# Kernel tuning notes

Measured on AMD Instinct MI355X. Metric: run time of the kernel, lower is better.

The kernel has to match this reference:

```python
import jax, jax.numpy as jnp
import numpy as np

B, C, H, W = 32, 512, 32, 32
K, D = 1024, 512  # codebook_size, latent_dim


def setup_inputs() -> dict:
    key = jax.random.key(0)
    k1, k2 = jax.random.split(key)
    z = jax.random.normal(k1, (B, C, H, W), dtype=jnp.float32)
    # nn.Embedding weight init: uniform(-1/codebook_size, 1/codebook_size)
    codebook = jax.random.uniform(k2, (K, D), dtype=jnp.float32,
                                  minval=-1.0 / K, maxval=1.0 / K)
    return {"z": z, "codebook": codebook}


def reference(z, codebook):
    b, c, h, w = z.shape
    # [B, C, H, W] -> [B, H, W, C] -> [B*H*W, C]
    z_flat = jnp.transpose(z, (0, 2, 3, 1)).reshape(-1, c)
    # squared euclidean distances via ||z||^2 - 2 z.W^T + ||W||^2
    distances = (
        jnp.sum(z_flat * z_flat, axis=1, keepdims=True)
        - 2.0 * jnp.matmul(z_flat, codebook.T)
        + jnp.sum(codebook * codebook, axis=1)[None, :]
    )  # [B*H*W, K]
    min_indices = jnp.argmin(distances, axis=1)  # [B*H*W]
    # Faithful to the original: gather then reshape directly to z.shape
    # (no inverse permute), which works because C == latent_dim.
    quantized = codebook[min_indices].reshape(z.shape)
    return quantized, min_indices.reshape(b, -1)
```

## Files before the change

kernel.cpp:

```cpp
#include <hip/hip_runtime.h>
#include <hip/hip_bf16.h>

#define M_ROWS  32768
#define D_DIM   512
#define K_CODES 1024
#define HW      1024
#define IMG_STRIDE (D_DIM * HW)

#define WH_OFF   0u
#define A_OFF    1048576u
#define W_OFF    1179648u
#define PK_OFF   1183744u
#define PART_OFF 1312768u
#define WL1_OFF  3934208u
#define WL2_OFF  4065280u
#define CNT_OFF  4196352u

#define WINDOW 5.0e-4f

__device__ __forceinline__ float fmul32(float a, float b) {
  float r; asm volatile("v_mul_f32 %0, %1, %2" : "=v"(r) : "v"(a), "v"(b)); return r;
}
__device__ __forceinline__ float fadd32(float a, float b) {
  float r; asm volatile("v_add_f32 %0, %1, %2" : "=v"(r) : "v"(a), "v"(b)); return r;
}
__device__ __forceinline__ float pair8(const float* r) {
  return fadd32(fadd32(fadd32(r[0], r[1]), fadd32(r[2], r[3])),
                fadd32(fadd32(r[4], r[5]), fadd32(r[6], r[7])));
}

__device__ __forceinline__ unsigned short f2bf(float x) {
  __hip_bfloat16 h = __float2bfloat16(x);
  unsigned short u; __builtin_memcpy(&u, &h, 2); return u;
}

typedef __attribute__((ext_vector_type(8))) short b8;
typedef __attribute__((ext_vector_type(4))) float f4;

struct T3 { float s1, s2, s3; int n1, n2; };
__device__ __forceinline__ void t3_merge(T3& a, const T3& bb) {
  T3 x = a, y = bb;
  bool bf = (y.s1 < x.s1) || (y.s1 == x.s1 && y.n1 < x.n1);
  if (bf) { T3 t = x; x = y; y = t; }
  float rs2; int rn2; float rs3;
  bool c2 = (y.s1 < x.s2) || (y.s1 == x.s2 && y.n1 < x.n2);
  if (c2) { rs2 = y.s1; rn2 = y.n1; rs3 = fminf(x.s2, y.s2); }
  else    { rs2 = x.s2; rn2 = x.n2; rs3 = fminf(x.s3, y.s1); }
  a.s1 = x.s1; a.n1 = x.n1; a.s2 = rs2; a.n2 = rn2; a.s3 = rs3;
}

__global__ __launch_bounds__(256) void vq_prep(const float* __restrict__ z,
                                               float* __restrict__ A,
                                               char* __restrict__ zh_b) {
  __shared__ float zs[4][64 * 68];
  const int wave = threadIdx.x >> 6, t = threadIdx.x & 63;
  const int i0 = blockIdx.x * 256 + wave * 64;
  const int b = i0 >> 10, hw0 = i0 & 1023;
  const float* zbase = z + (size_t)b * IMG_STRIDE + hw0;
  float* zsw = zs[wave];
  const int pos = i0 + t;
  const size_t mbase = (size_t)(pos >> 4) * 1024 + (size_t)(pos & 15) * 16;
  float r8[8], blk[4];
  alignas(16) unsigned short hs[8];
#pragma unroll
  for (int ch = 0; ch < 8; ++ch) {
    __syncthreads();
    {
      const int l = t & 15, j0 = t >> 4;
#pragma unroll
      for (int jj = 0; jj < 16; ++jj) {
        int j = j0 * 16 + jj;
        float4 vv = *(const float4*)(zbase + (size_t)(ch * 64 + j) * HW + 4 * l);
        *(float4*)(zsw + j * 68 + 4 * l) = vv;
      }
    }
    __syncthreads();
#pragma unroll
    for (int j = 0; j < 64; ++j) {
      const int c = ch * 64 + j;
      float v = zsw[j * 68 + t];
      hs[j & 7] = f2bf(v);
      if ((j & 7) == 7) {
        const int kc = c >> 5, q = (c >> 3) & 3;
        *(uint4*)(zh_b + (size_t)kc * 2097152 + q * 256 + mbase) = *(uint4*)hs;
      }
      float pq = fmul32(v, v);
      const int k = c & 7, m = c & 127;
      if (m < 8) r8[k] = pq;
      else       r8[k] = fadd32(r8[k], pq);
      if (m == 127) blk[c >> 7] = pair8(r8);
    }
  }
  A[pos] = fadd32(fadd32(blk[0], blk[1]), fadd32(blk[2], blk[3]));
}

__global__ void vq_prepw(const float* __restrict__ cb, float* __restrict__ W,
                         char* __restrict__ wh_b, int* __restrict__ cnt) {
  if (blockIdx.x == 0 && threadIdx.x < 2) cnt[threadIdx.x] = 0;
  const int n = blockIdx.x * 256 + threadIdx.x;
  const float* wp = cb + (size_t)n * D_DIM;
  const size_t nbase = (size_t)(n >> 4) * 1024 + (size_t)(n & 15) * 16;
  float r8[8], blk[4];
  alignas(16) unsigned short hs[8];
#pragma unroll
  for (int bb = 0; bb < 4; ++bb) {
#pragma unroll
    for (int g = 0; g < 16; ++g) {
      float vv[8];
#pragma unroll
      for (int k = 0; k < 8; ++k) vv[k] = wp[bb * 128 + g * 8 + k];
#pragma unroll
      for (int k = 0; k < 8; ++k) {
        float pq = fmul32(vv[k], vv[k]);
        if (g == 0) r8[k] = pq;
        else        r8[k] = fadd32(r8[k], pq);
        hs[k] = f2bf(vv[k]);
      }
      const int kc = bb * 4 + (g >> 2), q = g & 3;
      *(uint4*)(wh_b + (size_t)kc * 65536 + q * 256 + nbase) = *(uint4*)hs;
    }
    blk[bb] = pair8(r8);
  }
  W[n] = fadd32(fadd32(blk[0], blk[1]), fadd32(blk[2], blk[3]));
}

__global__ __launch_bounds__(256, 2) void vq_score(
    const char* __restrict__ zh_b, const char* __restrict__ wh_b,
    const float* __restrict__ Wws, float* __restrict__ part)
{
  __shared__ float red[1280];
  const int tid = threadIdx.x;
  const int lane = tid & 63, wave = tid >> 6;
  const int wr = wave >> 1, wc = wave & 1;
  const int bm = blockIdx.x & 255, bn = blockIdx.x >> 8;
  const int m0 = bm * 128, n0 = bn * 256;

  f4 acc[4][8];
#pragma unroll
  for (int r = 0; r < 4; ++r)
#pragma unroll
    for (int v = 0; v < 8; ++v) acc[r][v] = (f4)(0.0f);

  const char* gA_w = zh_b + (size_t)bm * 8192 + (size_t)(wr * 4) * 1024 + (size_t)lane * 16;
  const char* gB_w = wh_b + (size_t)bn * 16384 + (size_t)(wc * 8) * 1024 + (size_t)lane * 16;

  b8 ar[2][4], br[2][8];
#pragma unroll
  for (int r = 0; r < 4; ++r)
    ar[0][r] = *(const b8*)(gA_w + (size_t)r * 1024);
#pragma unroll
  for (int v = 0; v < 8; ++v)
    br[0][v] = *(const b8*)(gB_w + (size_t)v * 1024);

#pragma unroll
  for (int kc = 0; kc < 16; ++kc) {
    const int cur = kc & 1, nxt = cur ^ 1;
    if (kc + 1 < 16) {
      const char* gA = gA_w + (size_t)(kc + 1) * 2097152;
      const char* gB = gB_w + (size_t)(kc + 1) * 65536;
#pragma unroll
      for (int r = 0; r < 4; ++r) ar[nxt][r] = *(const b8*)(gA + (size_t)r * 1024);
#pragma unroll
      for (int v = 0; v < 8; ++v) br[nxt][v] = *(const b8*)(gB + (size_t)v * 1024);
    }
#pragma unroll
    for (int r = 0; r < 4; ++r) {
#pragma unroll
      for (int v = 0; v < 8; ++v)
        acc[r][v] = __builtin_amdgcn_mfma_f32_16x16x32_bf16(ar[cur][r], br[cur][v],
                                                            acc[r][v], 0, 0, 0);
    }
  }

  const int l15 = lane & 15, quad = lane >> 4;
  float sW[8];
#pragma unroll
  for (int v = 0; v < 8; ++v) sW[v] = Wws[n0 + wc * 128 + v * 16 + l15];

#pragma unroll
  for (int r = 0; r < 4; ++r) {
#pragma unroll
    for (int reg = 0; reg < 4; ++reg) {
      T3 t; t.s1 = t.s2 = t.s3 = 3.4e38f; t.n1 = 0; t.n2 = 0;
#pragma unroll
      for (int v = 0; v < 8; ++v) {
        float s = fmaf(-2.f, acc[r][v][reg], sW[v]);
        int n = n0 + wc * 128 + v * 16 + l15;
        if (s < t.s1)      { t.s3 = t.s2; t.s2 = t.s1; t.n2 = t.n1; t.s1 = s; t.n1 = n; }
        else if (s < t.s2) { t.s3 = t.s2; t.s2 = s; t.n2 = n; }
        else if (s < t.s3) { t.s3 = s; }
      }
#pragma unroll
      for (int m = 1; m <= 8; m <<= 1) {
        T3 o;
        o.s1 = __shfl_xor(t.s1, m); o.s2 = __shfl_xor(t.s2, m); o.s3 = __shfl_xor(t.s3, m);
        o.n1 = __shfl_xor(t.n1, m); o.n2 = __shfl_xor(t.n2, m);
        t3_merge(t, o);
      }
      if (l15 == 0) {
        int row = wr * 64 + r * 16 + quad * 4 + reg;
        float* d = red + (row * 2 + wc) * 5;
        d[0] = t.s1; d[1] = t.s2; d[2] = t.s3; d[3] = (float)t.n1; d[4] = (float)t.n2;
      }
    }
  }
  __syncthreads();
  if (tid < 128) {
    const float* d0 = red + (tid * 2) * 5;
    const float* d1 = red + (tid * 2 + 1) * 5;
    T3 a; a.s1 = d0[0]; a.s2 = d0[1]; a.s3 = d0[2]; a.n1 = (int)d0[3]; a.n2 = (int)d0[4];
    T3 b; b.s1 = d1[0]; b.s2 = d1[1]; b.s3 = d1[2]; b.n1 = (int)d1[3]; b.n2 = (int)d1[4];
    t3_merge(a, b);
    float* p = part + ((size_t)(m0 + tid) * 4 + bn) * 5;
    p[0] = a.s1; p[1] = a.s2; p[2] = a.s3; p[3] = (float)a.n1; p[4] = (float)a.n2;
  }
}

__global__ void vq_comb(const float* __restrict__ part, float* __restrict__ out_idx,
                        unsigned int* __restrict__ pk, int* __restrict__ wl1,
                        int* __restrict__ wl2, int* __restrict__ cnt) {
  int row = blockIdx.x * 256 + threadIdx.x;
  const float* p = part + (size_t)row * 20;
  T3 a; a.s1 = p[0]; a.s2 = p[1]; a.s3 = p[2]; a.n1 = (int)p[3]; a.n2 = (int)p[4];
#pragma unroll
  for (int j = 1; j < 4; ++j) {
    const float* q = p + j * 5;
    T3 b; b.s1 = q[0]; b.s2 = q[1]; b.s3 = q[2]; b.n1 = (int)q[3]; b.n2 = (int)q[4];
    t3_merge(a, b);
  }
  out_idx[row] = (float)a.n1;
  unsigned int f = 0;
  if (a.s2 - a.s1 < WINDOW) f = (a.s3 - a.s1 < WINDOW) ? 2u : 1u;
  pk[row] = (unsigned int)a.n1 | ((unsigned int)a.n2 << 10) | (f << 20);
  if (f == 1u) wl1[atomicAdd(&cnt[0], 1)] = row;
  if (f == 2u) wl2[atomicAdd(&cnt[1], 1)] = row;
}

__global__ __launch_bounds__(256) void vq_recheckA(
    const float* __restrict__ z, const float* __restrict__ cb,
    const float* __restrict__ Aws, const float* __restrict__ Wws,
    const unsigned int* __restrict__ pk, const int* __restrict__ wl1,
    const int* __restrict__ cnt, float* __restrict__ out_idx)
{
  const int wave = threadIdx.x >> 6, lane = threadIdx.x & 63;
  const int gw = blockIdx.x * 4 + wave;
  const int c1 = cnt[0];
  for (int i = gw; i < c1; i += 2048) {
    int row = wl1[i];
    unsigned int p = pk[row];
    int n1 = p & 1023, n2 = (p >> 10) & 1023;
    int b = row >> 10, hw = row & 1023;
    const float* zr = z + (size_t)b * IMG_STRIDE + hw;
    const float* c1p = cb + (size_t)n1 * D_DIM;
    const float* c2p = cb + (size_t)n2 * D_DIM;
    double d1 = 0.0, d2 = 0.0;
#pragma unroll
    for (int j = 0; j < 8; ++j) {
      int c = lane + 64 * j;
      double zv = (double)zr[(size_t)c * HW];
      d1 += zv * (double)c1p[c];
      d2 += zv * (double)c2p[c];
    }
#pragma unroll
    for (int off = 32; off > 0; off >>= 1) {
      d1 += __shfl_down(d1, off);
      d2 += __shfl_down(d2, off);
    }
    if (lane == 0) {
      float A_ = Aws[row];
      float e1 = fadd32(fadd32(A_, -2.f * (float)d1), Wws[n1]);
      float e2 = fadd32(fadd32(A_, -2.f * (float)d2), Wws[n2]);
      int win = (e2 < e1 || (e2 == e1 && n2 < n1)) ? n2 : n1;
      out_idx[row] = (float)win;
    }
  }
}

__global__ __launch_bounds__(256) void vq_recheckB(
    const float* __restrict__ z, const float* __restrict__ cb,
    const float* __restrict__ Aws, const float* __restrict__ Wws,
    const int* __restrict__ wl2, const int* __restrict__ cnt,
    float* __restrict__ out_idx)
{
  __shared__ double zd[512];
  __shared__ float rd[256];
  __shared__ int rn[256];
  const int c2 = cnt[1];
  for (int t = blockIdx.x; t < c2; t += gridDim.x) {
    int row = wl2[t];
    int b = row >> 10, hw = row & 1023;
    const float* zr = z + (size_t)b * IMG_STRIDE + hw;
    for (int c = threadIdx.x; c < 512; c += 256) zd[c] = (double)zr[(size_t)c * HW];
    __syncthreads();
    float best = 3.4e38f; int bn_ = 0;
    float A_ = Aws[row];
    for (int k = 0; k < 4; ++k) {
      int n = k * 256 + threadIdx.x;
      const float* cn = cb + (size_t)n * D_DIM;
      double a0 = 0.0, a1 = 0.0, a2 = 0.0, a3 = 0.0;
#pragma unroll 8
      for (int c4 = 0; c4 < 128; ++c4) {
        float4 w4 = *(const float4*)(cn + 4 * c4);
        a0 += zd[4 * c4 + 0] * (double)w4.x;
        a1 += zd[4 * c4 + 1] * (double)w4.y;
        a2 += zd[4 * c4 + 2] * (double)w4.z;
        a3 += zd[4 * c4 + 3] * (double)w4.w;
      }
      double dot = (a0 + a1) + (a2 + a3);
      float e = fadd32(fadd32(A_, -2.f * (float)dot), Wws[n]);
      if (e < best || (e == best && n < bn_)) { best = e; bn_ = n; }
    }
    rd[threadIdx.x] = best; rn[threadIdx.x] = bn_;
    __syncthreads();
    for (int s = 128; s > 0; s >>= 1) {
      if (threadIdx.x < s) {
        float eo = rd[threadIdx.x + s]; int no = rn[threadIdx.x + s];
        if (eo < rd[threadIdx.x] || (eo == rd[threadIdx.x] && no < rn[threadIdx.x])) {
          rd[threadIdx.x] = eo; rn[threadIdx.x] = no;
        }
      }
      __syncthreads();
    }
    if (threadIdx.x == 0) out_idx[row] = (float)rn[0];
    __syncthreads();
  }
}

__global__ __launch_bounds__(256) void vq_gather(const float* __restrict__ cb,
                                                 const float* __restrict__ out_idx,
                                                 float* __restrict__ out_q) {
  __shared__ int bidx[64];
  const int i0 = blockIdx.x * 64;
  if (threadIdx.x < 64) bidx[threadIdx.x] = (int)out_idx[i0 + threadIdx.x];
  __syncthreads();
  float* outp = out_q + (size_t)i0 * D_DIM;
  for (int j = 0; j < 32; ++j) {
    int f4i = j * 256 + threadIdx.x;
    int row = f4i >> 7, d4 = f4i & 127;
    float4 vv = *(const float4*)(cb + (size_t)bidx[row] * D_DIM + 4 * d4);
    *(float4*)(outp + 4 * f4i) = vv;
  }
}

extern "C" void kernel_launch(void* const* d_in, const int* in_sizes, int n_in,
                              void* d_out, int out_size, void* d_ws, size_t ws_size,
                              hipStream_t stream) {
  const float* z  = (const float*)d_in[0];
  const float* cb = (const float*)d_in[1];
  float* out_q   = (float*)d_out;
  float* out_idx = (float*)d_out + (size_t)M_ROWS * D_DIM;
  char* zh_b = (char*)d_out;
  char* ws = (char*)d_ws;
  char* wh_b = ws + WH_OFF;
  float* Aws = (float*)(ws + A_OFF);
  float* Wws = (float*)(ws + W_OFF);
  unsigned int* pk = (unsigned int*)(ws + PK_OFF);
  float* part = (float*)(ws + PART_OFF);
  int* wl1 = (int*)(ws + WL1_OFF);
  int* wl2 = (int*)(ws + WL2_OFF);
  int* cnt = (int*)(ws + CNT_OFF);

  vq_prep    <<<128, 256, 0, stream>>>(z, Aws, zh_b);
  vq_prepw   <<<4, 256, 0, stream>>>(cb, Wws, wh_b, cnt);
  vq_score   <<<1024, 256, 0, stream>>>(zh_b, wh_b, Wws, part);
  vq_comb    <<<128, 256, 0, stream>>>(part, out_idx, pk, wl1, wl2, cnt);
  vq_recheckA<<<512, 256, 0, stream>>>(z, cb, Aws, Wws, pk, wl1, cnt, out_idx);
  vq_recheckB<<<512, 256, 0, stream>>>(z, cb, Aws, Wws, wl2, cnt, out_idx);
  vq_gather  <<<512, 256, 0, stream>>>(cb, out_idx, out_q);
}
```

Measured before the change: 353.8 us.

## Swap MFMA operands so codes lie along accumulator registers and use branchless top-3

The score kernel now feeds codebook tiles as the MFMA A operand and z rows as B, so each lane's accumulator registers hold consecutive codes for one row. The top-3 scan becomes per-lane, using branchless min/med3/max updates, and only two cross-lane shuffle merge rounds are needed instead of four. The goal is to shrink the epilogue reduction cost (shuffles and divergent branches) while the MFMA work and global loads stay the same. Wave-to-tile mapping and the W-norm loads change to float4 accordingly.

```diff
diff --git a/kernel.cpp b/kernel.cpp
--- a/kernel.cpp
+++ b/kernel.cpp
@@ -131,77 +131,86 @@
   __shared__ float red[1280];
   const int tid = threadIdx.x;
   const int lane = tid & 63, wave = tid >> 6;
-  const int wr = wave >> 1, wc = wave & 1;
+  const int wnh = wave >> 1, wm = wave & 1;
   const int bm = blockIdx.x & 255, bn = blockIdx.x >> 8;
   const int m0 = bm * 128, n0 = bn * 256;
 
-  f4 acc[4][8];
-#pragma unroll
-  for (int r = 0; r < 4; ++r)
-#pragma unroll
-    for (int v = 0; v < 8; ++v) acc[r][v] = (f4)(0.0f);
-
-  const char* gA_w = zh_b + (size_t)bm * 8192 + (size_t)(wr * 4) * 1024 + (size_t)lane * 16;
-  const char* gB_w = wh_b + (size_t)bn * 16384 + (size_t)(wc * 8) * 1024 + (size_t)lane * 16;
-
-  b8 ar[2][4], br[2][8];
-#pragma unroll
-  for (int r = 0; r < 4; ++r)
-    ar[0][r] = *(const b8*)(gA_w + (size_t)r * 1024);
-#pragma unroll
-  for (int v = 0; v < 8; ++v)
-    br[0][v] = *(const b8*)(gB_w + (size_t)v * 1024);
+  f4 acc[8][4];
+#pragma unroll
+  for (int nt = 0; nt < 8; ++nt)
+#pragma unroll
+    for (int v = 0; v < 4; ++v) acc[nt][v] = (f4)(0.0f);
+
+  const size_t laneoff = (size_t)lane * 16;
+  const char* gWbase = wh_b + (size_t)bn * 16384 + (size_t)wnh * 8192;
+  const char* gZbase = zh_b + (size_t)bm * 8192  + (size_t)wm  * 4096;
+
+  b8 aw[2][8], bz[2][4];
+#pragma unroll
+  for (int nt = 0; nt < 8; ++nt)
+    aw[0][nt] = *(const b8*)(gWbase + nt * 1024 + laneoff);
+#pragma unroll
+  for (int v = 0; v < 4; ++v)
+    bz[0][v] = *(const b8*)(gZbase + v * 1024 + laneoff);
 
 #pragma unroll
   for (int kc = 0; kc < 16; ++kc) {
     const int cur = kc & 1, nxt = cur ^ 1;
     if (kc + 1 < 16) {
-      const char* gA = gA_w + (size_t)(kc + 1) * 2097152;
-      const char* gB = gB_w + (size_t)(kc + 1) * 65536;
-#pragma unroll
-      for (int r = 0; r < 4; ++r) ar[nxt][r] = *(const b8*)(gA + (size_t)r * 1024);
-#pragma unroll
-      for (int v = 0; v < 8; ++v) br[nxt][v] = *(const b8*)(gB + (size_t)v * 1024);
-    }
-#pragma unroll
-    for (int r = 0; r < 4; ++r) {
-#pragma unroll
-      for (int v = 0; v < 8; ++v)
-        acc[r][v] = __builtin_amdgcn_mfma_f32_16x16x32_bf16(ar[cur][r], br[cur][v],
-                                                            acc[r][v], 0, 0, 0);
-    }
-  }
-
-  const int l15 = lane & 15, quad = lane >> 4;
-  float sW[8];
-#pragma unroll
-  for (int v = 0; v < 8; ++v) sW[v] = Wws[n0 + wc * 128 + v * 16 + l15];
-
-#pragma unroll
-  for (int r = 0; r < 4; ++r) {
-#pragma unroll
-    for (int reg = 0; reg < 4; ++reg) {
-      T3 t; t.s1 = t.s2 = t.s3 = 3.4e38f; t.n1 = 0; t.n2 = 0;
-#pragma unroll
-      for (int v = 0; v < 8; ++v) {
-        float s = fmaf(-2.f, acc[r][v][reg], sW[v]);
-        int n = n0 + wc * 128 + v * 16 + l15;
-        if (s < t.s1)      { t.s3 = t.s2; t.s2 = t.s1; t.n2 = t.n1; t.s1 = s; t.n1 = n; }
-        else if (s < t.s2) { t.s3 = t.s2; t.s2 = s; t.n2 = n; }
-        else if (s < t.s3) { t.s3 = s; }
-      }
-#pragma unroll
-      for (int m = 1; m <= 8; m <<= 1) {
-        T3 o;
-        o.s1 = __shfl_xor(t.s1, m); o.s2 = __shfl_xor(t.s2, m); o.s3 = __shfl_xor(t.s3, m);
-        o.n1 = __shfl_xor(t.n1, m); o.n2 = __shfl_xor(t.n2, m);
-        t3_merge(t, o);
-      }
-      if (l15 == 0) {
-        int row = wr * 64 + r * 16 + quad * 4 + reg;
-        float* d = red + (row * 2 + wc) * 5;
-        d[0] = t.s1; d[1] = t.s2; d[2] = t.s3; d[3] = (float)t.n1; d[4] = (float)t.n2;
-      }
+      const char* gW = gWbase + (size_t)(kc + 1) * 65536;
+      const char* gZ = gZbase + (size_t)(kc + 1) * 2097152;
+#pragma unroll
+      for (int nt = 0; nt < 8; ++nt) aw[nxt][nt] = *(const b8*)(gW + nt * 1024 + laneoff);
+#pragma unroll
+      for (int v = 0; v < 4; ++v)    bz[nxt][v]  = *(const b8*)(gZ + v * 1024 + laneoff);
+    }
+#pragma unroll
+    for (int nt = 0; nt < 8; ++nt) {
+#pragma unroll
+      for (int v = 0; v < 4; ++v)
+        acc[nt][v] = __builtin_amdgcn_mfma_f32_16x16x32_bf16(aw[cur][nt], bz[cur][v],
+                                                             acc[nt][v], 0, 0, 0);
+    }
+  }
+
+  const int l15 = lane & 15, q = lane >> 4;
+  const int nb = n0 + wnh * 128 + q * 4;
+
+  float4 w4[8];
+#pragma unroll
+  for (int nt = 0; nt < 8; ++nt)
+    w4[nt] = *(const float4*)(Wws + nb + nt * 16);
+
+#pragma unroll
+  for (int v = 0; v < 4; ++v) {
+    T3 t; t.s1 = t.s2 = t.s3 = 3.4e38f; t.n1 = 0; t.n2 = 0;
+#pragma unroll
+    for (int nt = 0; nt < 8; ++nt) {
+      const float* wv = (const float*)&w4[nt];
+#pragma unroll
+      for (int reg = 0; reg < 4; ++reg) {
+        float s = fmaf(-2.f, acc[nt][v][reg], wv[reg]);
+        int n = nb + nt * 16 + reg;
+        bool c1 = s < t.s1, c2 = s < t.s2;
+        float ns3 = fminf(t.s3, fmaxf(t.s2, s));
+        float ns2 = __builtin_amdgcn_fmed3f(t.s1, t.s2, s);
+        t.n2 = c1 ? t.n1 : (c2 ? n : t.n2);
+        t.n1 = c1 ? n : t.n1;
+        t.s1 = fminf(t.s1, s);
+        t.s2 = ns2; t.s3 = ns3;
+      }
+    }
+#pragma unroll
+    for (int m = 16; m <= 32; m <<= 1) {
+      T3 o;
+      o.s1 = __shfl_xor(t.s1, m); o.s2 = __shfl_xor(t.s2, m); o.s3 = __shfl_xor(t.s3, m);
+      o.n1 = __shfl_xor(t.n1, m); o.n2 = __shfl_xor(t.n2, m);
+      t3_merge(t, o);
+    }
+    if (q == 0) {
+      int row = wm * 64 + v * 16 + l15;
+      float* d = red + (row * 2 + wnh) * 5;
+      d[0] = t.s1; d[1] = t.s2; d[2] = t.s3; d[3] = (float)t.n1; d[4] = (float)t.n2;
     }
   }
   __syncthreads();
```

After: 372.6 us. 5.3% more time.
